# Optimization experiments

Hardware: AMD Instinct MI355X
Metric: run time of the kernel (lower is better)

The kernel has to match this reference:

```python
import jax, jax.numpy as jnp
import numpy as np

B, T, C = 16, 2048, 1024
HEAD = 64

def setup_inputs() -> dict:
    key = jax.random.key(0)
    kx, kq, kk, kv = jax.random.split(key, 4)
    x = jax.random.normal(kx, (B, T, C), dtype=jnp.float32)
    s = 1.0 / np.sqrt(C)
    Wq = jax.random.normal(kq, (C, HEAD), dtype=jnp.float32) * s
    Wk = jax.random.normal(kk, (C, HEAD), dtype=jnp.float32) * s
    Wv = jax.random.normal(kv, (C, HEAD), dtype=jnp.float32) * s
    return {"x": x, "Wq": Wq, "Wk": Wk, "Wv": Wv}

def reference(x, Wq, Wk, Wv):
    Bb, Tt, Cc = x.shape
    q = jnp.einsum('btc,ch->bth', x, Wq)  # [B,T,H]
    k = jnp.einsum('btc,ch->bth', x, Wk)
    v = jnp.einsum('btc,ch->bth', x, Wv)
    # NOTE: source scales by C**-0.5 (n_embd), not head_size**-0.5
    scores = jnp.einsum('bth,bsh->bts', q, k) * (Cc ** -0.5)  # [B,T,T]
    causal = jnp.tril(jnp.ones((Tt, Tt), dtype=bool))
    scores = jnp.where(causal, scores, -jnp.inf)
    attn = jax.nn.softmax(scores, axis=-1)  # dropout p=0 -> identity
    out = jnp.einsum('bts,bsh->bth', attn, v)  # [B,T,H]
    return out
```

## Files before the change

kernel.cpp:

```cpp
#include <hip/hip_runtime.h>

typedef __bf16 bf16;
typedef __bf16 bf16x2 __attribute__((ext_vector_type(2)));
typedef __bf16 bf16x4 __attribute__((ext_vector_type(4)));
typedef __bf16 bf16x8 __attribute__((ext_vector_type(8)));
typedef float f32x4 __attribute__((ext_vector_type(4)));

#define TT_ 2048
#define CC_ 1024
#define HH_ 64

#define SCALE2 0.045084221f

static __device__ __forceinline__ unsigned pack_bf16(float a, float b) {
    union { bf16x2 h; unsigned u; } z;
    z.h = bf16x2{(bf16)a, (bf16)b};
    return z.u;
}
static __device__ __forceinline__ void plswap32(unsigned &a, unsigned &b) {
    asm("v_permlane32_swap_b32 %0, %1" : "+v"(a), "+v"(b));
}
static __device__ __forceinline__ void plswap16(unsigned &a, unsigned &b) {
    asm("v_permlane16_swap_b32 %0, %1" : "+v"(a), "+v"(b));
}

__global__ __launch_bounds__(256) void prep_w(const float* __restrict__ Wq,
                                              const float* __restrict__ Wk,
                                              const float* __restrict__ Wv,
                                              bf16* __restrict__ Wt) {
    __shared__ bf16 Ls[64 * 65];
    const int m  = blockIdx.x >> 4;
    const int k0 = (blockIdx.x & 15) * 64;
    const float* W = (m == 0) ? Wq : (m == 1) ? Wk : Wv;
    const int tid = threadIdx.x;
    #pragma unroll
    for (int j = 0; j < 4; ++j) {
        int idx = tid + 256 * j;
        int r   = idx >> 4;
        int c4  = (idx & 15) * 4;
        float4 w = *(const float4*)&W[(size_t)(k0 + r) * HH_ + c4];
        Ls[r * 65 + c4 + 0] = (bf16)w.x;
        Ls[r * 65 + c4 + 1] = (bf16)w.y;
        Ls[r * 65 + c4 + 2] = (bf16)w.z;
        Ls[r * 65 + c4 + 3] = (bf16)w.w;
    }
    __syncthreads();
    #pragma unroll
    for (int j = 0; j < 4; ++j) {
        int idx = tid + 256 * j;
        int n   = idx >> 4;
        int kc  = (idx & 15) * 4;
        bf16x4 v;
        #pragma unroll
        for (int i = 0; i < 4; ++i) v[i] = Ls[(kc + i) * 65 + n];
        *(bf16x4*)&Wt[m * 65536 + n * 1024 + k0 + kc] = v;
    }
}

__global__ __launch_bounds__(256) void qkv_kernel(const float* __restrict__ x,
                                                  const bf16* __restrict__ Wt,
                                                  bf16* __restrict__ qb,
                                                  bf16* __restrict__ kb,
                                                  bf16* __restrict__ vt) {
    __shared__ __align__(16) bf16 Xs[2][64 * 72];
    const int tid  = threadIdx.x;
    const int wave = tid >> 6;
    const int lane = tid & 15;
    const int quad = (tid & 63) >> 4;
    const int m0   = blockIdx.x * 64;

    f32x4 acc[4][3];
    #pragma unroll
    for (int i = 0; i < 4; ++i)
        #pragma unroll
        for (int j = 0; j < 3; ++j) acc[i][j] = f32x4{0.f, 0.f, 0.f, 0.f};

    const int srow = tid >> 4;
    const int scol = (tid & 15) * 4;

    float4 xr[4];
    #pragma unroll
    for (int rr = 0; rr < 4; ++rr)
        xr[rr] = *(const float4*)&x[(size_t)(m0 + srow + rr * 16) * CC_ + scol];
    #pragma unroll
    for (int rr = 0; rr < 4; ++rr) {
        bf16x4 bv = {(bf16)xr[rr].x, (bf16)xr[rr].y, (bf16)xr[rr].z, (bf16)xr[rr].w};
        *(bf16x4*)&Xs[0][(srow + rr * 16) * 72 + scol] = bv;
    }

    for (int kbi = 0; kbi < 16; ++kbi) {
        const int cur = kbi & 1;
        const int k0  = kbi * 64;
        __syncthreads();
        if (kbi < 15) {
            #pragma unroll
            for (int rr = 0; rr < 4; ++rr)
                xr[rr] = *(const float4*)&x[(size_t)(m0 + srow + rr * 16) * CC_ + k0 + 64 + scol];
        }
        bf16x8 bfr[2][3];
        #pragma unroll
        for (int step = 0; step < 2; ++step)
            #pragma unroll
            for (int ct = 0; ct < 3; ++ct)
                bfr[step][ct] = *(const bf16x8*)&Wt[(size_t)(wave * 48 + ct * 16 + lane) * 1024 + k0 + step * 32 + quad * 8];
        bf16x8 afr[2][4];
        #pragma unroll
        for (int step = 0; step < 2; ++step)
            #pragma unroll
            for (int rt = 0; rt < 4; ++rt)
                afr[step][rt] = *(const bf16x8*)&Xs[cur][(rt * 16 + lane) * 72 + step * 32 + quad * 8];
        #pragma unroll
        for (int step = 0; step < 2; ++step)
            #pragma unroll
            for (int ct = 0; ct < 3; ++ct)
                #pragma unroll
                for (int rt = 0; rt < 4; ++rt)
                    acc[rt][ct] = __builtin_amdgcn_mfma_f32_16x16x32_bf16(afr[step][rt], bfr[step][ct], acc[rt][ct], 0, 0, 0);
        if (kbi < 15) {
            #pragma unroll
            for (int rr = 0; rr < 4; ++rr) {
                bf16x4 bv = {(bf16)xr[rr].x, (bf16)xr[rr].y, (bf16)xr[rr].z, (bf16)xr[rr].w};
                *(bf16x4*)&Xs[cur ^ 1][(srow + rr * 16) * 72 + scol] = bv;
            }
        }
    }

    const int bb = m0 >> 11;
    const int t0 = m0 & 2047;
    __syncthreads();
    #pragma unroll
    for (int ct = 0; ct < 3; ++ct) {
        int c0 = wave * 48 + ct * 16;
        if (c0 < 128) {
            bf16* outp = (c0 < 64) ? qb : kb;
            int h = (c0 & 63) + lane;
            #pragma unroll
            for (int rt = 0; rt < 4; ++rt)
                #pragma unroll
                for (int r = 0; r < 4; ++r)
                    outp[(size_t)(m0 + rt * 16 + quad * 4 + r) * HH_ + h] = (bf16)acc[rt][ct][r];
        } else {
            int h = (c0 - 128) + lane;
            #pragma unroll
            for (int rt = 0; rt < 4; ++rt)
                #pragma unroll
                for (int r = 0; r < 4; ++r)
                    Xs[0][(rt * 16 + quad * 4 + r) * 72 + h] = (bf16)acc[rt][ct][r];
        }
    }
    __syncthreads();
    {
        int h  = tid >> 2;
        int tc = (tid & 3) * 16;
        bf16x8 v0, v1;
        #pragma unroll
        for (int i = 0; i < 8; ++i) v0[i] = Xs[0][(tc + i) * 72 + h];
        #pragma unroll
        for (int i = 0; i < 8; ++i) v1[i] = Xs[0][(tc + 8 + i) * 72 + h];
        bf16* dst = &vt[(size_t)bb * HH_ * TT_ + (size_t)h * TT_ + t0 + tc];
        *(bf16x8*)dst = v0;
        *(bf16x8*)(dst + 8) = v1;
    }
}

__global__ __launch_bounds__(256, 4) void attn_kernel(const bf16* __restrict__ qb,
                                                      const bf16* __restrict__ kb,
                                                      const bf16* __restrict__ vt,
                                                      bf16* __restrict__ PO,
                                                      float* __restrict__ PL) {
    __shared__ __align__(16) bf16 Ks[128 * 72];
    __shared__ __align__(16) bf16 Vs[64 * 136];

    const int tid  = threadIdx.x;
    const int wave = tid >> 6;
    const int lane = tid & 15;
    const int quad = (tid & 63) >> 4;
    const int idx = blockIdx.x;
    const int bb  = blockIdx.y;
    int seg, qi;
    if (idx < 32)      { seg = 0; qi = idx; }
    else if (idx < 56) { seg = 1; qi = idx - 24; }
    else if (idx < 72) { seg = 2; qi = idx - 40; }
    else               { seg = 3; qi = idx - 48; }
    const int q0    = qi * 64;
    const int nch   = (seg < (qi >> 3)) ? 4 : (((qi & 7) + 2) >> 1);
    const int diagc = (seg == (qi >> 3)) ? nch - 1 : -1;
    const int s00   = seg * 512;

    const int qrow  = q0 + wave * 16;
    const int qg    = qrow + lane;
    const int qmaxw = qrow + 15;

    const int krow = tid >> 3, kc8 = (tid & 7) * 8;
    const int vh   = tid >> 4, vc8 = (tid & 15) * 8;
    const bf16* kp = kb + (size_t)(bb * TT_ + s00 + krow) * HH_ + kc8;
    const bf16* vp = vt + (size_t)bb * HH_ * TT_ + (size_t)vh * TT_ + s00 + vc8;

    bf16x8 kr[4], vvr[4];
    #pragma unroll
    for (int j = 0; j < 4; ++j) kr[j]  = *(const bf16x8*)&kp[(size_t)j * 32 * HH_];
    #pragma unroll
    for (int j = 0; j < 4; ++j) vvr[j] = *(const bf16x8*)&vp[j * 16 * TT_];

    bf16x8 aq[2];
    #pragma unroll
    for (int step = 0; step < 2; ++step)
        aq[step] = *(const bf16x8*)&qb[(size_t)(bb * TT_ + qg) * HH_ + step * 32 + quad * 8];

    f32x4 o_acc[4];
    #pragma unroll
    for (int ht = 0; ht < 4; ++ht) o_acc[ht] = f32x4{0.f, 0.f, 0.f, 0.f};
    float lsum = 0.f;

    for (int c = 0; c < nch; ++c) {
        const int s0 = s00 + c * 128;
        __syncthreads();
        #pragma unroll
        for (int j = 0; j < 4; ++j) *(bf16x8*)&Ks[(krow + 32 * j) * 72 + kc8] = kr[j];
        #pragma unroll
        for (int j = 0; j < 4; ++j) *(bf16x8*)&Vs[(vh + 16 * j) * 136 + vc8]  = vvr[j];
        __syncthreads();
        if (c + 1 < nch) {
            #pragma unroll
            for (int j = 0; j < 4; ++j)
                kr[j] = *(const bf16x8*)&kp[(size_t)((c + 1) * 128 + j * 32) * HH_];
            #pragma unroll
            for (int j = 0; j < 4; ++j)
                vvr[j] = *(const bf16x8*)&vp[(c + 1) * 128 + j * 16 * TT_];
        }

        const bool msk = (c == diagc);
        #pragma unroll
        for (int w = 0; w < 4; ++w) {
            if (msk && (s0 + w * 32 > qmaxw)) continue;
            const bool haveB = !msk || (s0 + w * 32 + 16 <= qmaxw);

            f32x4 sA = {0.f, 0.f, 0.f, 0.f};
            f32x4 sB = {0.f, 0.f, 0.f, 0.f};
            {
                bf16x8 ak0 = *(const bf16x8*)&Ks[(w * 32 + lane) * 72 + quad * 8];
                bf16x8 ak1 = *(const bf16x8*)&Ks[(w * 32 + lane) * 72 + 32 + quad * 8];
                sA = __builtin_amdgcn_mfma_f32_16x16x32_bf16(ak0, aq[0], sA, 0, 0, 0);
                sA = __builtin_amdgcn_mfma_f32_16x16x32_bf16(ak1, aq[1], sA, 0, 0, 0);
            }
            if (haveB) {
                bf16x8 bk0 = *(const bf16x8*)&Ks[(w * 32 + 16 + lane) * 72 + quad * 8];
                bf16x8 bk1 = *(const bf16x8*)&Ks[(w * 32 + 16 + lane) * 72 + 32 + quad * 8];
                sB = __builtin_amdgcn_mfma_f32_16x16x32_bf16(bk0, aq[0], sB, 0, 0, 0);
                sB = __builtin_amdgcn_mfma_f32_16x16x32_bf16(bk1, aq[1], sB, 0, 0, 0);
            }

            const int kA0 = s0 + w * 32 + quad * 4;
            float eA[4], eB[4];
            #pragma unroll
            for (int r = 0; r < 4; ++r) {
                float e = __builtin_amdgcn_exp2f(sA[r] * SCALE2);
                if (msk && (kA0 + r > qg)) e = 0.f;
                eA[r] = e;
            }
            if (haveB) {
                #pragma unroll
                for (int r = 0; r < 4; ++r) {
                    float e = __builtin_amdgcn_exp2f(sB[r] * SCALE2);
                    if (msk && (kA0 + 16 + r > qg)) e = 0.f;
                    eB[r] = e;
                }
            } else {
                #pragma unroll
                for (int r = 0; r < 4; ++r) eB[r] = 0.f;
            }
            lsum += ((eA[0] + eA[1]) + (eA[2] + eA[3])) +
                    ((eB[0] + eB[1]) + (eB[2] + eB[3]));

            unsigned d0 = pack_bf16(eA[0], eA[1]);
            unsigned d1 = pack_bf16(eA[2], eA[3]);
            unsigned d2 = pack_bf16(eB[0], eB[1]);
            unsigned d3 = pack_bf16(eB[2], eB[3]);
            plswap32(d0, d2);
            plswap16(d0, d2);
            plswap32(d1, d3);
            plswap16(d1, d3);
            union { unsigned u[4]; bf16x8 v; } apu;
            apu.u[0] = d0; apu.u[1] = d1; apu.u[2] = d2; apu.u[3] = d3;

            #pragma unroll
            for (int ht = 0; ht < 4; ++ht) {
                bf16x8 bv = *(const bf16x8*)&Vs[(ht * 16 + lane) * 136 + w * 32 + quad * 8];
                o_acc[ht] = __builtin_amdgcn_mfma_f32_16x16x32_bf16(apu.v, bv, o_acc[ht], 0, 0, 0);
            }
        }
    }

    const size_t p = (size_t)bb * 80 + idx;
    #pragma unroll
    for (int ht = 0; ht < 4; ++ht)
        #pragma unroll
        for (int r = 0; r < 4; ++r)
            PO[p * 4096 + (size_t)(wave * 16 + quad * 4 + r) * 64 + ht * 16 + lane] = (bf16)o_acc[ht][r];

    float l = lsum;
    l += __shfl_xor(l, 16);
    l += __shfl_xor(l, 32);
    if (quad == 0) PL[p * 64 + wave * 16 + lane] = l;
}

__global__ __launch_bounds__(256) void combine_kernel(const bf16* __restrict__ PO,
                                                      const float* __restrict__ PL,
                                                      float* __restrict__ out) {
    const int qi = blockIdx.x, bb = blockIdx.y;
    const int tid = threadIdx.x;
    const int r  = tid >> 2;
    const int cb = (tid & 3) * 16;
    const int ns = (qi >> 3) + 1;
    const int off[4] = {0, 32, 56, 72};

    float acc[16];
    #pragma unroll
    for (int i = 0; i < 16; ++i) acc[i] = 0.f;
    float l = 0.f;
    for (int s = 0; s < ns; ++s) {
        const size_t p = (size_t)bb * 80 + off[s] + qi - 8 * s;
        l += PL[p * 64 + r];
        const bf16* po = &PO[p * 4096 + (size_t)r * 64 + cb];
        bf16x8 a0 = *(const bf16x8*)po;
        bf16x8 a1 = *(const bf16x8*)(po + 8);
        #pragma unroll
        for (int i = 0; i < 8; ++i) { acc[i] += (float)a0[i]; acc[8 + i] += (float)a1[i]; }
    }
    const float inv = 1.0f / l;
    float* dst = &out[(size_t)(bb * TT_ + qi * 64 + r) * HH_ + cb];
    #pragma unroll
    for (int v = 0; v < 4; ++v) {
        float4 o = {acc[v * 4] * inv, acc[v * 4 + 1] * inv, acc[v * 4 + 2] * inv, acc[v * 4 + 3] * inv};
        *(float4*)(dst + v * 4) = o;
    }
}

extern "C" void kernel_launch(void* const* d_in, const int* in_sizes, int n_in,
                              void* d_out, int out_size, void* d_ws, size_t ws_size,
                              hipStream_t stream) {
    const float* x  = (const float*)d_in[0];
    const float* Wq = (const float*)d_in[1];
    const float* Wk = (const float*)d_in[2];
    const float* Wv = (const float*)d_in[3];
    float* out = (float*)d_out;

    char* ws = (char*)d_ws;
    bf16*  qb = (bf16*)(ws);
    bf16*  kb = (bf16*)(ws + 4194304);
    bf16*  vt = (bf16*)(ws + 8388608);
    bf16*  Wt = (bf16*)(ws + 12582912);
    bf16*  PO = (bf16*)(ws + 12976128);
    float* PL = (float*)(ws + 23461888);

    prep_w<<<48, 256, 0, stream>>>(Wq, Wk, Wv, Wt);
    qkv_kernel<<<512, 256, 0, stream>>>(x, Wt, qb, kb, vt);
    attn_kernel<<<dim3(80, 16), 256, 0, stream>>>(qb, kb, vt, PO, PL);
    combine_kernel<<<dim3(32, 16), 256, 0, stream>>>(PO, PL, out);
}
```

Measured before the change: 246.7 us.

## Software-pipeline QKV projection loads two steps ahead and raise MFMA wave priority

The QKV projection loop is restructured into a macro-unrolled pair of steps with ping-pong register buffers, so x tiles are prefetched two k-blocks ahead and weight fragments one block ahead. This hides global load latency behind the MFMA work. It also adds launch_bounds(256,2) as an occupancy hint, and wraps the attention MFMA sections in s_setprio so waves issuing matrix ops get scheduling priority. The costs are higher register pressure from the duplicated buffers and possible register spills under the occupancy bound.

```diff
diff --git a/kernel.cpp b/kernel.cpp
--- a/kernel.cpp
+++ b/kernel.cpp
@@ -57,11 +57,49 @@
     }
 }
 
-__global__ __launch_bounds__(256) void qkv_kernel(const float* __restrict__ x,
-                                                  const bf16* __restrict__ Wt,
-                                                  bf16* __restrict__ qb,
-                                                  bf16* __restrict__ kb,
-                                                  bf16* __restrict__ vt) {
+#define QKV_STEP(KBI, BU, BP, XLD, XWR)                                        \
+    {                                                                          \
+        const int k0 = (KBI) * 64;                                             \
+        __syncthreads();                                                       \
+        if ((KBI) < 14) {                                                      \
+            _Pragma("unroll")                                                  \
+            for (int rr = 0; rr < 4; ++rr)                                     \
+                XLD[rr] = *(const float4*)&x[(size_t)(m0 + srow + rr * 16) * CC_ + k0 + 128 + scol]; \
+        }                                                                      \
+        if ((KBI) < 15) {                                                      \
+            _Pragma("unroll")                                                  \
+            for (int step = 0; step < 2; ++step)                               \
+                _Pragma("unroll")                                              \
+                for (int ct = 0; ct < 3; ++ct)                                 \
+                    BP[step][ct] = *(const bf16x8*)&Wt[(size_t)(wave * 48 + ct * 16 + lane) * 1024 + k0 + 64 + step * 32 + quad * 8]; \
+        }                                                                      \
+        bf16x8 afr[2][4];                                                      \
+        _Pragma("unroll")                                                      \
+        for (int step = 0; step < 2; ++step)                                   \
+            _Pragma("unroll")                                                  \
+            for (int rt = 0; rt < 4; ++rt)                                     \
+                afr[step][rt] = *(const bf16x8*)&Xs[(KBI) & 1][(rt * 16 + lane) * 72 + step * 32 + quad * 8]; \
+        _Pragma("unroll")                                                      \
+        for (int step = 0; step < 2; ++step)                                   \
+            _Pragma("unroll")                                                  \
+            for (int ct = 0; ct < 3; ++ct)                                     \
+                _Pragma("unroll")                                              \
+                for (int rt = 0; rt < 4; ++rt)                                 \
+                    acc[rt][ct] = __builtin_amdgcn_mfma_f32_16x16x32_bf16(afr[step][rt], BU[step][ct], acc[rt][ct], 0, 0, 0); \
+        if ((KBI) < 15) {                                                      \
+            _Pragma("unroll")                                                  \
+            for (int rr = 0; rr < 4; ++rr) {                                   \
+                bf16x4 bv = {(bf16)XWR[rr].x, (bf16)XWR[rr].y, (bf16)XWR[rr].z, (bf16)XWR[rr].w}; \
+                *(bf16x4*)&Xs[((KBI) + 1) & 1][(srow + rr * 16) * 72 + scol] = bv; \
+            }                                                                  \
+        }                                                                      \
+    }
+
+__global__ __launch_bounds__(256, 2) void qkv_kernel(const float* __restrict__ x,
+                                                     const bf16* __restrict__ Wt,
+                                                     bf16* __restrict__ qb,
+                                                     bf16* __restrict__ kb,
+                                                     bf16* __restrict__ vt) {
     __shared__ __align__(16) bf16 Xs[2][64 * 72];
     const int tid  = threadIdx.x;
     const int wave = tid >> 6;
@@ -78,51 +116,31 @@
     const int srow = tid >> 4;
     const int scol = (tid & 15) * 4;
 
-    float4 xr[4];
+    {
+        float4 x0[4];
+        #pragma unroll
+        for (int rr = 0; rr < 4; ++rr)
+            x0[rr] = *(const float4*)&x[(size_t)(m0 + srow + rr * 16) * CC_ + scol];
+        #pragma unroll
+        for (int rr = 0; rr < 4; ++rr) {
+            bf16x4 bv = {(bf16)x0[rr].x, (bf16)x0[rr].y, (bf16)x0[rr].z, (bf16)x0[rr].w};
+            *(bf16x4*)&Xs[0][(srow + rr * 16) * 72 + scol] = bv;
+        }
+    }
+    float4 xS0[4], xS1[4];
     #pragma unroll
     for (int rr = 0; rr < 4; ++rr)
-        xr[rr] = *(const float4*)&x[(size_t)(m0 + srow + rr * 16) * CC_ + scol];
-    #pragma unroll
-    for (int rr = 0; rr < 4; ++rr) {
-        bf16x4 bv = {(bf16)xr[rr].x, (bf16)xr[rr].y, (bf16)xr[rr].z, (bf16)xr[rr].w};
-        *(bf16x4*)&Xs[0][(srow + rr * 16) * 72 + scol] = bv;
-    }
-
-    for (int kbi = 0; kbi < 16; ++kbi) {
-        const int cur = kbi & 1;
-        const int k0  = kbi * 64;
-        __syncthreads();
-        if (kbi < 15) {
-            #pragma unroll
-            for (int rr = 0; rr < 4; ++rr)
-                xr[rr] = *(const float4*)&x[(size_t)(m0 + srow + rr * 16) * CC_ + k0 + 64 + scol];
-        }
-        bf16x8 bfr[2][3];
-        #pragma unroll
-        for (int step = 0; step < 2; ++step)
-            #pragma unroll
-            for (int ct = 0; ct < 3; ++ct)
-                bfr[step][ct] = *(const bf16x8*)&Wt[(size_t)(wave * 48 + ct * 16 + lane) * 1024 + k0 + step * 32 + quad * 8];
-        bf16x8 afr[2][4];
-        #pragma unroll
-        for (int step = 0; step < 2; ++step)
-            #pragma unroll
-            for (int rt = 0; rt < 4; ++rt)
-                afr[step][rt] = *(const bf16x8*)&Xs[cur][(rt * 16 + lane) * 72 + step * 32 + quad * 8];
-        #pragma unroll
-        for (int step = 0; step < 2; ++step)
-            #pragma unroll
-            for (int ct = 0; ct < 3; ++ct)
-                #pragma unroll
-                for (int rt = 0; rt < 4; ++rt)
-                    acc[rt][ct] = __builtin_amdgcn_mfma_f32_16x16x32_bf16(afr[step][rt], bfr[step][ct], acc[rt][ct], 0, 0, 0);
-        if (kbi < 15) {
-            #pragma unroll
-            for (int rr = 0; rr < 4; ++rr) {
-                bf16x4 bv = {(bf16)xr[rr].x, (bf16)xr[rr].y, (bf16)xr[rr].z, (bf16)xr[rr].w};
-                *(bf16x4*)&Xs[cur ^ 1][(srow + rr * 16) * 72 + scol] = bv;
-            }
-        }
+        xS1[rr] = *(const float4*)&x[(size_t)(m0 + srow + rr * 16) * CC_ + 64 + scol];
+    bf16x8 bfrA[2][3], bfrB[2][3];
+    #pragma unroll
+    for (int step = 0; step < 2; ++step)
+        #pragma unroll
+        for (int ct = 0; ct < 3; ++ct)
+            bfrA[step][ct] = *(const bf16x8*)&Wt[(size_t)(wave * 48 + ct * 16 + lane) * 1024 + step * 32 + quad * 8];
+
+    for (int kb2 = 0; kb2 < 16; kb2 += 2) {
+        QKV_STEP(kb2,     bfrA, bfrB, xS0, xS1)
+        QKV_STEP(kb2 + 1, bfrB, bfrA, xS1, xS0)
     }
 
     const int bb = m0 >> 11;
@@ -237,6 +255,7 @@
 
             f32x4 sA = {0.f, 0.f, 0.f, 0.f};
             f32x4 sB = {0.f, 0.f, 0.f, 0.f};
+            __builtin_amdgcn_s_setprio(1);
             {
                 bf16x8 ak0 = *(const bf16x8*)&Ks[(w * 32 + lane) * 72 + quad * 8];
                 bf16x8 ak1 = *(const bf16x8*)&Ks[(w * 32 + lane) * 72 + 32 + quad * 8];
@@ -249,6 +268,7 @@
                 sB = __builtin_amdgcn_mfma_f32_16x16x32_bf16(bk0, aq[0], sB, 0, 0, 0);
                 sB = __builtin_amdgcn_mfma_f32_16x16x32_bf16(bk1, aq[1], sB, 0, 0, 0);
             }
+            __builtin_amdgcn_s_setprio(0);
 
             const int kA0 = s0 + w * 32 + quad * 4;
             float eA[4], eB[4];
@@ -283,11 +303,13 @@
             union { unsigned u[4]; bf16x8 v; } apu;
             apu.u[0] = d0; apu.u[1] = d1; apu.u[2] = d2; apu.u[3] = d3;
 
+            __builtin_amdgcn_s_setprio(1);
             #pragma unroll
             for (int ht = 0; ht < 4; ++ht) {
                 bf16x8 bv = *(const bf16x8*)&Vs[(ht * 16 + lane) * 136 + w * 32 + quad * 8];
                 o_acc[ht] = __builtin_amdgcn_mfma_f32_16x16x32_bf16(apu.v, bv, o_acc[ht], 0, 0, 0);
             }
+            __builtin_amdgcn_s_setprio(0);
         }
     }
 
```

Measured after the change: 241.8 us. -2.0%, faster.
